# Kernel tuning notes

Hardware: AMD Instinct MI355X
Metric: run time of the kernel (lower is better)

Reference implementation:

```python
import jax, jax.numpy as jnp
import numpy as np

D_MODEL = 1024
N_HEADS = 16
TOP_FACTOR = 5


def setup_inputs() -> dict:
    key = jax.random.key(0)
    ks = jax.random.split(key, 9)
    B, L, D = 2, 4096, D_MODEL
    s = 0.02
    return {
        "x": jax.random.normal(ks[0], (B, L, D), dtype=jnp.float32),
        "Wq": jax.random.normal(ks[1], (D, D), dtype=jnp.float32) * s,
        "bq": jnp.zeros((D,), dtype=jnp.float32),
        "Wk": jax.random.normal(ks[2], (D, D), dtype=jnp.float32) * s,
        "bk": jnp.zeros((D,), dtype=jnp.float32),
        "Wv": jax.random.normal(ks[3], (D, D), dtype=jnp.float32) * s,
        "bv": jnp.zeros((D,), dtype=jnp.float32),
        "Wo": jax.random.normal(ks[4], (D, D), dtype=jnp.float32) * s,
        "bo": jnp.zeros((D,), dtype=jnp.float32),
    }


def reference(x, Wq, bq, Wk, bk, Wv, bv, Wo, bo):
    B, L, D = x.shape
    H = N_HEADS
    hd = D // H
    BH = B * H
    top_u = max(1, L // TOP_FACTOR)

    def proj(W, b):
        # [B,L,D] -> [B*H, L, hd] (matches view + transpose(1,2) in torch)
        y = x @ W.T + b
        return y.reshape(B, L, H, hd).transpose(0, 2, 1, 3).reshape(BH, L, hd)

    Q = proj(Wq, bq)
    K = proj(Wk, bk)
    V = proj(Wv, bv)

    # select top-u queries per (batch,head) by L2 norm
    query_norms = jnp.linalg.norm(Q, axis=2)              # [BH, L]
    _, top_idx = jax.lax.top_k(query_norms, top_u)        # [BH, top_u]
    Q_sel = jnp.take_along_axis(Q, top_idx[:, :, None], axis=1)  # [BH, u, hd]

    scale = 1.0 / (hd ** 0.5)
    scores = jnp.einsum('bud,bld->bul', Q_sel, K) * scale  # [BH, u, L]
    attn = jax.nn.softmax(scores, axis=-1)
    out_sel = jnp.einsum('bul,bld->bud', attn, V)          # [BH, u, hd]

    # scatter selected outputs back; non-selected rows stay zero
    out_full = jnp.zeros((BH, L, hd), dtype=x.dtype)
    out_full = out_full.at[jnp.arange(BH)[:, None], top_idx].set(out_sel)

    out = out_full.reshape(B, H, L, hd).transpose(0, 2, 1, 3).reshape(B, L, D)
    return out @ Wo.T + bo
```

## Files before the change

kernel.cpp:

```cpp
#include <hip/hip_runtime.h>
#include <cstddef>
#include <cstdint>

constexpr int LSEQ = 4096;
constexpr int DM   = 1024;
constexpr int HD   = 64;
constexpr int BHT  = 32;
constexpr int TOPU = 819;
constexpr int MROWS = 8192;
constexpr int NSEG = 4;

typedef unsigned short u16;
typedef __attribute__((ext_vector_type(8))) short short8v;
typedef __attribute__((ext_vector_type(4))) short short4v;
typedef __attribute__((ext_vector_type(4))) float f32x4;

__device__ __forceinline__ u16 f2bf(float f) {
  uint32_t u = __float_as_uint(f);
  u += 0x7fffu + ((u >> 16) & 1u);
  return (u16)(u >> 16);
}
__device__ __forceinline__ float bf2f(u16 h) {
  return __uint_as_float(((uint32_t)h) << 16);
}

__device__ __forceinline__ void gl16(const void* g, void* l) {
  __builtin_amdgcn_global_load_lds(
      (const __attribute__((address_space(1))) void*)g,
      (__attribute__((address_space(3))) void*)l, 16, 0, 0);
}

__device__ __forceinline__ void inv_swz(int S, int& R, int& C) {
  const int R0 = ((S >> 5) ^ (S >> 7)) & 1;
  const int R1 = (S >> 6) & 1;
  R = ((S >> 6) << 1) | R0;
  C = (((S >> 3) & 1) ^ R0) | ((((S >> 4) & 1) ^ R1) << 1);
}

__device__ __forceinline__ void split3_body(const float* src, u16* p1, u16* p2,
                                            u16* p3, int i) {
  const float4 a = *reinterpret_cast<const float4*>(src + (size_t)i * 8);
  const float4 b = *reinterpret_cast<const float4*>(src + (size_t)i * 8 + 4);
  float e[8] = {a.x, a.y, a.z, a.w, b.x, b.y, b.z, b.w};
  short8v v1, v2, v3;
  #pragma unroll
  for (int j = 0; j < 8; ++j) {
    u16 h1 = f2bf(e[j]);        float r1 = e[j] - bf2f(h1);
    u16 h2 = f2bf(r1);          float r2 = r1 - bf2f(h2);
    u16 h3 = f2bf(r2);
    v1[j] = (short)h1; v2[j] = (short)h2; v3[j] = (short)h3;
  }
  *reinterpret_cast<short8v*>(p1 + (size_t)i * 8) = v1;
  *reinterpret_cast<short8v*>(p2 + (size_t)i * 8) = v2;
  *reinterpret_cast<short8v*>(p3 + (size_t)i * 8) = v3;
}

__device__ __forceinline__ void conv_body(const float* src, u16* dst, int i) {
  const float4 a = *reinterpret_cast<const float4*>(src + (size_t)i * 8);
  const float4 b = *reinterpret_cast<const float4*>(src + (size_t)i * 8 + 4);
  short8v v;
  v[0] = (short)f2bf(a.x); v[1] = (short)f2bf(a.y);
  v[2] = (short)f2bf(a.z); v[3] = (short)f2bf(a.w);
  v[4] = (short)f2bf(b.x); v[5] = (short)f2bf(b.y);
  v[6] = (short)f2bf(b.z); v[7] = (short)f2bf(b.w);
  *reinterpret_cast<short8v*>(dst + (size_t)i * 8) = v;
}

__global__ __launch_bounds__(256) void prep_all(
    const float* __restrict__ x,  const float* __restrict__ Wq,
    const float* __restrict__ Wk, const float* __restrict__ Wv,
    const float* __restrict__ Wo,
    u16* __restrict__ x1, u16* __restrict__ x2, u16* __restrict__ x3,
    u16* __restrict__ wq1, u16* __restrict__ wq2, u16* __restrict__ wq3,
    u16* __restrict__ Wkb, u16* __restrict__ Wvb, u16* __restrict__ Wob)
{
  const int NX = MROWS * DM / 8;
  const int NW = DM * DM / 8;
  int i = blockIdx.x * 256 + threadIdx.x;
  if (i < NX)  { split3_body(x,  x1,  x2,  x3,  i); return; }
  i -= NX;
  if (i < NW)  { split3_body(Wq, wq1, wq2, wq3, i); return; }
  i -= NW;
  if (i < NW)  { conv_body(Wk, Wkb, i); return; }
  i -= NW;
  if (i < NW)  { conv_body(Wv, Wvb, i); return; }
  i -= NW;
  if (i < NW)  { conv_body(Wo, Wob, i); }
}

__device__ __forceinline__ void proj_q_body(
    u16* smem,
    const u16* __restrict__ X1, const u16* __restrict__ X2, const u16* __restrict__ X3,
    const u16* __restrict__ W1, const u16* __restrict__ W2, const u16* __restrict__ W3,
    const float* __restrict__ bias, float* __restrict__ Y,
    float* __restrict__ norms, int bx, int ny)
{
  u16* As[3] = {smem, smem + 4096, smem + 8192};
  u16* Bs[3] = {smem + 12288, smem + 16384, smem + 20480};
  const int tid = threadIdx.x;
  const int m0 = bx * 128, n0 = ny * 128;
  const int wid = tid >> 6, lane = tid & 63;
  const int wr = (wid >> 1) * 64, wc = (wid & 1) * 64;
  const int c = lane & 15, G = lane >> 4;

  int Rr[2], Cr[2];
  #pragma unroll
  for (int rr = 0; rr < 2; ++rr) inv_swz((tid + rr * 256) * 8, Rr[rr], Cr[rr]);

  f32x4 acc[4][4];
  #pragma unroll
  for (int mt = 0; mt < 4; ++mt)
    #pragma unroll
    for (int nt = 0; nt < 4; ++nt)
      acc[mt][nt] = (f32x4){0.f, 0.f, 0.f, 0.f};

  for (int k0 = 0; k0 < DM; k0 += 32) {
    #pragma unroll
    for (int rr = 0; rr < 2; ++rr) {
      const size_t goA = (size_t)(m0 + Rr[rr]) * DM + k0 + Cr[rr] * 8;
      const size_t goB = (size_t)(n0 + Rr[rr]) * DM + k0 + Cr[rr] * 8;
      const int lb = wid * 512 + rr * 2048;
      gl16(X1 + goA, As[0] + lb);
      gl16(X2 + goA, As[1] + lb);
      gl16(X3 + goA, As[2] + lb);
      gl16(W1 + goB, Bs[0] + lb);
      gl16(W2 + goB, Bs[1] + lb);
      gl16(W3 + goB, Bs[2] + lb);
    }
    __syncthreads();

    short8v bf[3][4];
    #pragma unroll
    for (int nt = 0; nt < 4; ++nt) {
      const int n = wc + nt * 16 + c;
      const int eo = (n * 32 + G * 8) ^ ((n & 7) << 3);
      bf[0][nt] = *reinterpret_cast<const short8v*>(Bs[0] + eo);
      bf[1][nt] = *reinterpret_cast<const short8v*>(Bs[1] + eo);
      bf[2][nt] = *reinterpret_cast<const short8v*>(Bs[2] + eo);
    }
    #pragma unroll
    for (int mt = 0; mt < 4; ++mt) {
      const int m = wr + mt * 16 + c;
      const int eo = (m * 32 + G * 8) ^ ((m & 7) << 3);
      short8v a1 = *reinterpret_cast<const short8v*>(As[0] + eo);
      short8v a2 = *reinterpret_cast<const short8v*>(As[1] + eo);
      short8v a3 = *reinterpret_cast<const short8v*>(As[2] + eo);
      #pragma unroll
      for (int nt = 0; nt < 4; ++nt) {
        acc[mt][nt] = __builtin_amdgcn_mfma_f32_16x16x32_bf16(a1, bf[0][nt], acc[mt][nt], 0, 0, 0);
        acc[mt][nt] = __builtin_amdgcn_mfma_f32_16x16x32_bf16(a1, bf[1][nt], acc[mt][nt], 0, 0, 0);
        acc[mt][nt] = __builtin_amdgcn_mfma_f32_16x16x32_bf16(a2, bf[0][nt], acc[mt][nt], 0, 0, 0);
        acc[mt][nt] = __builtin_amdgcn_mfma_f32_16x16x32_bf16(a2, bf[1][nt], acc[mt][nt], 0, 0, 0);
        acc[mt][nt] = __builtin_amdgcn_mfma_f32_16x16x32_bf16(a1, bf[2][nt], acc[mt][nt], 0, 0, 0);
        acc[mt][nt] = __builtin_amdgcn_mfma_f32_16x16x32_bf16(a3, bf[0][nt], acc[mt][nt], 0, 0, 0);
      }
    }
    __syncthreads();
  }

  float bb[4];
  #pragma unroll
  for (int nt = 0; nt < 4; ++nt) bb[nt] = bias[n0 + wc + nt * 16 + c];

  float ns[4][4];
  #pragma unroll
  for (int mt = 0; mt < 4; ++mt)
    #pragma unroll
    for (int r = 0; r < 4; ++r) ns[mt][r] = 0.f;

  #pragma unroll
  for (int mt = 0; mt < 4; ++mt) {
    #pragma unroll
    for (int nt = 0; nt < 4; ++nt) {
      const int n = n0 + wc + nt * 16 + c;
      const int h = n >> 6, d = n & 63;
      #pragma unroll
      for (int r = 0; r < 4; ++r) {
        const int m = m0 + wr + mt * 16 + G * 4 + r;
        const int b = m >> 12, l = m & (LSEQ - 1);
        const float val = acc[mt][nt][r] + bb[nt];
        Y[((size_t)((b << 4) + h) * LSEQ + l) * HD + d] = val;
        ns[mt][r] = fmaf(val, val, ns[mt][r]);
      }
    }
  }
  #pragma unroll
  for (int mt = 0; mt < 4; ++mt)
    #pragma unroll
    for (int r = 0; r < 4; ++r) {
      float v = ns[mt][r];
      v += __shfl_xor(v, 1); v += __shfl_xor(v, 2);
      v += __shfl_xor(v, 4); v += __shfl_xor(v, 8);
      ns[mt][r] = v;
    }
  if (c == 0) {
    const int h = (n0 + wc) >> 6;
    #pragma unroll
    for (int mt = 0; mt < 4; ++mt)
      #pragma unroll
      for (int r = 0; r < 4; ++r) {
        const int m = m0 + wr + mt * 16 + G * 4 + r;
        const int b = m >> 12, l = m & (LSEQ - 1);
        norms[(((size_t)((b << 4) + h)) << 12) + l] = ns[mt][r];
      }
  }
}

__device__ __forceinline__ void proj_kv_body(
    u16* smem, const u16* __restrict__ Xb, const u16* __restrict__ Wb,
    const float* __restrict__ bias, u16* __restrict__ Kb, u16* __restrict__ VgT,
    bool isV, int bx, int ny)
{
  u16* As = smem;
  u16* Bs = smem + 4096;
  const int tid = threadIdx.x;
  const int m0 = bx * 128, n0 = ny * 128;
  const int wid = tid >> 6, lane = tid & 63;
  const int wr = (wid >> 1) * 64, wc = (wid & 1) * 64;
  const int c = lane & 15, G = lane >> 4;

  int Rr[2], Cr[2];
  #pragma unroll
  for (int rr = 0; rr < 2; ++rr) inv_swz((tid + rr * 256) * 8, Rr[rr], Cr[rr]);

  f32x4 acc[4][4];
  #pragma unroll
  for (int mt = 0; mt < 4; ++mt)
    #pragma unroll
    for (int nt = 0; nt < 4; ++nt)
      acc[mt][nt] = (f32x4){0.f, 0.f, 0.f, 0.f};

  for (int k0 = 0; k0 < DM; k0 += 32) {
    #pragma unroll
    for (int rr = 0; rr < 2; ++rr) {
      const size_t goA = (size_t)(m0 + Rr[rr]) * DM + k0 + Cr[rr] * 8;
      const size_t goB = (size_t)(n0 + Rr[rr]) * DM + k0 + Cr[rr] * 8;
      const int lb = wid * 512 + rr * 2048;
      gl16(Xb + goA, As + lb);
      gl16(Wb + goB, Bs + lb);
    }
    __syncthreads();

    short8v af[4], bf[4];
    #pragma unroll
    for (int mt = 0; mt < 4; ++mt) {
      const int m = wr + mt * 16 + c;
      af[mt] = *reinterpret_cast<const short8v*>(As + ((m * 32 + G * 8) ^ ((m & 7) << 3)));
      const int n = wc + mt * 16 + c;
      bf[mt] = *reinterpret_cast<const short8v*>(Bs + ((n * 32 + G * 8) ^ ((n & 7) << 3)));
    }
    #pragma unroll
    for (int mt = 0; mt < 4; ++mt)
      #pragma unroll
      for (int nt = 0; nt < 4; ++nt)
        acc[mt][nt] = __builtin_amdgcn_mfma_f32_16x16x32_bf16(af[mt], bf[nt], acc[mt][nt], 0, 0, 0);
    __syncthreads();
  }

  float bb[4];
  #pragma unroll
  for (int nt = 0; nt < 4; ++nt) bb[nt] = bias[n0 + wc + nt * 16 + c];

  if (isV) {
    #pragma unroll
    for (int mt = 0; mt < 4; ++mt) {
      #pragma unroll
      for (int nt = 0; nt < 4; ++nt) {
        const int n = wc + nt * 16 + c;
        const int mloc = wr + mt * 16 + G * 4;
        short4v pv;
        #pragma unroll
        for (int r = 0; r < 4; ++r) pv[r] = (short)f2bf(acc[mt][nt][r] + bb[nt]);
        *reinterpret_cast<short4v*>(smem + n * 136 + mloc) = pv;
      }
    }
    __syncthreads();
    const int bb2 = m0 >> 12;
    const int ml0 = m0 & (LSEQ - 1);
    #pragma unroll
    for (int uu = 0; uu < 8; ++uu) {
      const int u = uu * 256 + tid;
      const int n = u >> 4, kg = u & 15;
      short8v vvv = *reinterpret_cast<const short8v*>(smem + n * 136 + kg * 8);
      const int h = (n0 + n) >> 6, d = (n0 + n) & 63;
      *reinterpret_cast<short8v*>(
          VgT + ((size_t)((bb2 << 4) + h) * HD + d) * LSEQ + ml0 + kg * 8) = vvv;
    }
  } else {
    #pragma unroll
    for (int mt = 0; mt < 4; ++mt) {
      #pragma unroll
      for (int nt = 0; nt < 4; ++nt) {
        const int n = n0 + wc + nt * 16 + c;
        const int h = n >> 6, d = n & 63;
        #pragma unroll
        for (int r = 0; r < 4; ++r) {
          const int m = m0 + wr + mt * 16 + G * 4 + r;
          const int b = m >> 12, l = m & (LSEQ - 1);
          Kb[((size_t)((b << 4) + h) * LSEQ + l) * HD + d] = f2bf(acc[mt][nt][r] + bb[nt]);
        }
      }
    }
  }
}

__global__ __launch_bounds__(256) void gemm_proj(
    const u16* __restrict__ X1, const u16* __restrict__ X2, const u16* __restrict__ X3,
    const u16* __restrict__ W1, const u16* __restrict__ W2, const u16* __restrict__ W3,
    const u16* __restrict__ Wkb, const u16* __restrict__ Wvb,
    const float* __restrict__ bq, const float* __restrict__ bk, const float* __restrict__ bv,
    float* __restrict__ Qb, float* __restrict__ norms,
    u16* __restrict__ Kb, u16* __restrict__ VgT, int y_off)
{
  __shared__ __align__(16) u16 smem[24576];
  const int by = blockIdx.y + y_off;
  const int bx = blockIdx.x;
  if (by < 8) {
    proj_q_body(smem, X1, X2, X3, W1, W2, W3, bq, Qb, norms, bx, by);
  } else if (by < 16) {
    proj_kv_body(smem, X1, Wvb, bv, Kb, VgT, true, bx, by - 8);
  } else {
    proj_kv_body(smem, X1, Wkb, bk, Kb, VgT, false, bx, by - 16);
  }
}

__global__ __launch_bounds__(256) void gemm_out(
    const u16* __restrict__ Xb, const u16* __restrict__ Wb,
    const float* __restrict__ bias, float* __restrict__ Y)
{
  __shared__ u16 As[128 * 32];
  __shared__ u16 Bs[128 * 32];
  const int tid = threadIdx.x;
  const int m0 = blockIdx.x * 128, n0 = blockIdx.y * 128;
  const int wid = tid >> 6, lane = tid & 63;
  const int wr = (wid >> 1) * 64, wc = (wid & 1) * 64;
  const int c = lane & 15, G = lane >> 4;

  int Rr[2], Cr[2];
  #pragma unroll
  for (int rr = 0; rr < 2; ++rr) inv_swz((tid + rr * 256) * 8, Rr[rr], Cr[rr]);

  f32x4 acc[4][4];
  #pragma unroll
  for (int mt = 0; mt < 4; ++mt)
    #pragma unroll
    for (int nt = 0; nt < 4; ++nt)
      acc[mt][nt] = (f32x4){0.f, 0.f, 0.f, 0.f};

  for (int k0 = 0; k0 < DM; k0 += 32) {
    #pragma unroll
    for (int rr = 0; rr < 2; ++rr) {
      const size_t goA = (size_t)(m0 + Rr[rr]) * DM + k0 + Cr[rr] * 8;
      const size_t goB = (size_t)(n0 + Rr[rr]) * DM + k0 + Cr[rr] * 8;
      const int lb = wid * 512 + rr * 2048;
      gl16(Xb + goA, As + lb);
      gl16(Wb + goB, Bs + lb);
    }
    __syncthreads();

    short8v af[4], bf[4];
    #pragma unroll
    for (int mt = 0; mt < 4; ++mt) {
      const int m = wr + mt * 16 + c;
      af[mt] = *reinterpret_cast<const short8v*>(As + ((m * 32 + G * 8) ^ ((m & 7) << 3)));
      const int n = wc + mt * 16 + c;
      bf[mt] = *reinterpret_cast<const short8v*>(Bs + ((n * 32 + G * 8) ^ ((n & 7) << 3)));
    }
    #pragma unroll
    for (int mt = 0; mt < 4; ++mt)
      #pragma unroll
      for (int nt = 0; nt < 4; ++nt)
        acc[mt][nt] = __builtin_amdgcn_mfma_f32_16x16x32_bf16(af[mt], bf[nt], acc[mt][nt], 0, 0, 0);
    __syncthreads();
  }

  float bb[4];
  #pragma unroll
  for (int nt = 0; nt < 4; ++nt) bb[nt] = bias[n0 + wc + nt * 16 + c];

  #pragma unroll
  for (int mt = 0; mt < 4; ++mt) {
    #pragma unroll
    for (int nt = 0; nt < 4; ++nt) {
      const int n = n0 + wc + nt * 16 + c;
      #pragma unroll
      for (int r = 0; r < 4; ++r) {
        const int m = m0 + wr + mt * 16 + G * 4 + r;
        Y[(size_t)m * DM + n] = acc[mt][nt][r] + bb[nt];
      }
    }
  }
}

__global__ __launch_bounds__(1024) void select_topk(
    const float* __restrict__ norms, int* __restrict__ top_idx)
{
  __shared__ unsigned int keys[LSEQ];
  __shared__ unsigned int hist[256];
  __shared__ unsigned int wsums[16];
  __shared__ unsigned int sh_b, sh_above;

  const int tid = threadIdx.x;
  const int bh = blockIdx.x;

  for (int l = tid; l < LSEQ; l += 1024)
    keys[l] = __float_as_uint(norms[bh * LSEQ + l]);
  __syncthreads();

  unsigned int prefix = 0, rem = TOPU, total_gt = 0;
  for (int shift = 24; shift >= 0; shift -= 8) {
    if (tid < 256) hist[tid] = 0;
    __syncthreads();
    for (int l = tid; l < LSEQ; l += 1024) {
      const unsigned int k = keys[l];
      const bool in = (shift == 24) || ((k >> (shift + 8)) == prefix);
      if (in) atomicAdd(&hist[(k >> shift) & 255], 1);
    }
    __syncthreads();
    if (tid == 0) {
      unsigned int cum = 0; int b = 255;
      for (; b > 0; --b) {
        const unsigned int h = hist[b];
        if (cum + h >= rem) break;
        cum += h;
      }
      sh_b = (unsigned int)b; sh_above = cum;
    }
    __syncthreads();
    prefix = (prefix << 8) | sh_b;
    total_gt += sh_above;
    rem -= sh_above;
    __syncthreads();
  }
  const unsigned int T = prefix;

  const int lane = tid & 63, wv = tid >> 6;
  const int l0 = tid * 4;

  {
    unsigned int flags = 0; int cnt = 0;
    #pragma unroll
    for (int j = 0; j < 4; ++j)
      if (keys[l0 + j] > T) { flags |= 1u << j; ++cnt; }
    int incl = cnt;
    #pragma unroll
    for (int off = 1; off < 64; off <<= 1) {
      int nv = __shfl_up(incl, off);
      if (lane >= off) incl += nv;
    }
    if (lane == 63) wsums[wv] = (unsigned int)incl;
    __syncthreads();
    if (tid == 0) {
      unsigned int run = 0;
      for (int w = 0; w < 16; ++w) { unsigned int t = wsums[w]; wsums[w] = run; run += t; }
    }
    __syncthreads();
    unsigned int pos = wsums[wv] + (unsigned int)(incl - cnt);
    #pragma unroll
    for (int j = 0; j < 4; ++j)
      if (flags & (1u << j)) top_idx[bh * TOPU + (pos++)] = l0 + j;
  }
  __syncthreads();

  {
    unsigned int flags = 0; int cnt = 0;
    #pragma unroll
    for (int j = 0; j < 4; ++j)
      if (keys[l0 + j] == T) { flags |= 1u << j; ++cnt; }
    int incl = cnt;
    #pragma unroll
    for (int off = 1; off < 64; off <<= 1) {
      int nv = __shfl_up(incl, off);
      if (lane >= off) incl += nv;
    }
    if (lane == 63) wsums[wv] = (unsigned int)incl;
    __syncthreads();
    if (tid == 0) {
      unsigned int run = 0;
      for (int w = 0; w < 16; ++w) { unsigned int t = wsums[w]; wsums[w] = run; run += t; }
    }
    __syncthreads();
    unsigned int r0 = wsums[wv] + (unsigned int)(incl - cnt);
    #pragma unroll
    for (int j = 0; j < 4; ++j)
      if (flags & (1u << j)) {
        if (r0 < rem) top_idx[bh * TOPU + total_gt + r0] = l0 + j;
        ++r0;
      }
  }
}

__global__ __launch_bounds__(256) void attn_mfma(
    const float* __restrict__ Qf, const u16* __restrict__ Kg,
    const u16* __restrict__ VgT, const int* __restrict__ tix,
    u16* __restrict__ OpartB, float* __restrict__ MLpart)
{
  __shared__ u16 Kc[128 * 64];
  __shared__ u16 Vt[64 * 128];
  __shared__ u16 Pt[4][16 * 136];

  const int tid = threadIdx.x;
  const int wid = tid >> 6, lane = tid & 63;
  const int c = lane & 15, G = lane >> 4;

  const int l = blockIdx.x;
  const int grp = l >> 3;
  const int bh = (grp / 52) * 8 + (l & 7);
  const int rem = grp % 52;
  const int qb = rem >> 2, ks = rem & 3;

  const size_t bhL = (size_t)bh * LSEQ;
  const int rglob = qb * 64 + wid * 16 + c;
  const int rowidx = (rglob < TOPU) ? tix[bh * TOPU + rglob] : -1;

  short8v qf[2];
  #pragma unroll
  for (int kf = 0; kf < 2; ++kf) {
    if (rowidx >= 0) {
      const float* qp = Qf + (bhL + rowidx) * HD + kf * 32 + G * 8;
      const float4 x0 = *reinterpret_cast<const float4*>(qp);
      const float4 x1 = *reinterpret_cast<const float4*>(qp + 4);
      short8v v;
      v[0] = (short)f2bf(x0.x * 0.125f); v[1] = (short)f2bf(x0.y * 0.125f);
      v[2] = (short)f2bf(x0.z * 0.125f); v[3] = (short)f2bf(x0.w * 0.125f);
      v[4] = (short)f2bf(x1.x * 0.125f); v[5] = (short)f2bf(x1.y * 0.125f);
      v[6] = (short)f2bf(x1.z * 0.125f); v[7] = (short)f2bf(x1.w * 0.125f);
      qf[kf] = v;
    } else {
      short8v v;
      #pragma unroll
      for (int j = 0; j < 8; ++j) v[j] = 0;
      qf[kf] = v;
    }
  }

  float m = -1e30f, lsum = 0.f;
  f32x4 oacc[4];
  #pragma unroll
  for (int dt = 0; dt < 4; ++dt) oacc[dt] = (f32x4){0.f, 0.f, 0.f, 0.f};

  const int ko0 = ks * (LSEQ / NSEG);
  const int wbase = (tid & ~63) * 8;
  for (int t = 0; t < LSEQ / NSEG / 128; ++t) {
    const int ko = ko0 + t * 128;
    #pragma unroll
    for (int uu = 0; uu < 4; ++uu) {
      const int S = (uu * 256 + tid) * 8;
      const int key = S >> 6, dgk = ((S >> 3) & 7) ^ (key & 7);
      gl16(Kg + (bhL + ko + key) * HD + dgk * 8, Kc + uu * 2048 + wbase);
      const int d = S >> 7, kgv = ((S >> 3) & 15) ^ (d & 7);
      gl16(VgT + ((size_t)bh * HD + d) * LSEQ + ko + kgv * 8, Vt + uu * 2048 + wbase);
    }
    __syncthreads();

    f32x4 sacc[8];
    __builtin_amdgcn_s_setprio(1);
    #pragma unroll
    for (int kt = 0; kt < 8; ++kt) {
      const int key = kt * 16 + c;
      short8v kb0 = *reinterpret_cast<const short8v*>(
          Kc + key * 64 + (((0 + G) ^ (key & 7)) << 3));
      short8v kb1 = *reinterpret_cast<const short8v*>(
          Kc + key * 64 + (((4 + G) ^ (key & 7)) << 3));
      f32x4 s = (f32x4){0.f, 0.f, 0.f, 0.f};
      s = __builtin_amdgcn_mfma_f32_16x16x32_bf16(kb0, qf[0], s, 0, 0, 0);
      s = __builtin_amdgcn_mfma_f32_16x16x32_bf16(kb1, qf[1], s, 0, 0, 0);
      sacc[kt] = s;
    }
    __builtin_amdgcn_s_setprio(0);

    float smax = -1e30f;
    #pragma unroll
    for (int kt = 0; kt < 8; ++kt) {
      float a0 = fmaxf(sacc[kt][0], sacc[kt][1]);
      float a1 = fmaxf(sacc[kt][2], sacc[kt][3]);
      smax = fmaxf(smax, fmaxf(a0, a1));
    }
    smax = fmaxf(smax, __shfl_xor(smax, 16));
    smax = fmaxf(smax, __shfl_xor(smax, 32));
    const float mnew = fmaxf(m, smax);
    const float corr = __expf(m - mnew);
    float ssum = 0.f;
    #pragma unroll
    for (int kt = 0; kt < 8; ++kt) {
      float p0 = __expf(sacc[kt][0] - mnew);
      float p1 = __expf(sacc[kt][1] - mnew);
      float p2 = __expf(sacc[kt][2] - mnew);
      float p3 = __expf(sacc[kt][3] - mnew);
      ssum += (p0 + p1) + (p2 + p3);
      short4v pv;
      pv[0] = (short)f2bf(p0); pv[1] = (short)f2bf(p1);
      pv[2] = (short)f2bf(p2); pv[3] = (short)f2bf(p3);
      *reinterpret_cast<short4v*>(&Pt[wid][c * 136 + kt * 16 + G * 4]) = pv;
    }
    ssum += __shfl_xor(ssum, 16);
    ssum += __shfl_xor(ssum, 32);
    lsum = lsum * corr + ssum;
    m = mnew;
    #pragma unroll
    for (int dt = 0; dt < 4; ++dt) oacc[dt] *= corr;

    __builtin_amdgcn_s_setprio(1);
    #pragma unroll
    for (int kf = 0; kf < 4; ++kf) {
      short8v pf = *reinterpret_cast<const short8v*>(
          &Pt[wid][c * 136 + kf * 32 + G * 8]);
      #pragma unroll
      for (int dt = 0; dt < 4; ++dt) {
        const int d = dt * 16 + c;
        short8v vf = *reinterpret_cast<const short8v*>(
            Vt + d * 128 + (((kf * 4 + G) ^ (d & 7)) << 3));
        oacc[dt] = __builtin_amdgcn_mfma_f32_16x16x32_bf16(vf, pf, oacc[dt], 0, 0, 0);
      }
    }
    __builtin_amdgcn_s_setprio(0);
    __syncthreads();
  }

  const int q = wid * 16 + c;
  const size_t pb = ((size_t)((bh * 13 + qb) * NSEG + ks)) * 64 + q;
  u16* op = OpartB + pb * 64;
  #pragma unroll
  for (int dt = 0; dt < 4; ++dt) {
    short4v o;
    o[0] = (short)f2bf(oacc[dt][0]); o[1] = (short)f2bf(oacc[dt][1]);
    o[2] = (short)f2bf(oacc[dt][2]); o[3] = (short)f2bf(oacc[dt][3]);
    *reinterpret_cast<short4v*>(op + dt * 16 + G * 4) = o;
  }
  if (G == 0) {
    MLpart[pb * 2]     = m;
    MLpart[pb * 2 + 1] = lsum;
  }
}

__global__ __launch_bounds__(256) void attn_combine(
    const u16* __restrict__ OpartB, const float* __restrict__ MLpart,
    const int* __restrict__ tix, u16* __restrict__ O1b)
{
  const int bq = blockIdx.x;
  const int bh = bq / 13, qb = bq % 13;
  const int tid = threadIdx.x;
  const int q = tid >> 2, dq = (tid & 3) * 16;
  const int rglob = qb * 64 + q;
  if (rglob >= TOPU) return;
  const int rowidx = tix[bh * TOPU + rglob];

  size_t p[NSEG];
  float mi[NSEG], li[NSEG];
  #pragma unroll
  for (int i = 0; i < NSEG; ++i) {
    p[i] = ((size_t)bq * NSEG + i) * 64 + q;
    mi[i] = MLpart[p[i] * 2];
    li[i] = MLpart[p[i] * 2 + 1];
  }
  float mx = fmaxf(fmaxf(mi[0], mi[1]), fmaxf(mi[2], mi[3]));
  float ci[NSEG], lsum = 0.f;
  #pragma unroll
  for (int i = 0; i < NSEG; ++i) { ci[i] = __expf(mi[i] - mx); lsum += li[i] * ci[i]; }
  const float linv = 1.0f / lsum;

  float acc[16];
  #pragma unroll
  for (int j = 0; j < 16; ++j) acc[j] = 0.f;
  #pragma unroll
  for (int i = 0; i < NSEG; ++i) {
    const u16* src = OpartB + p[i] * 64 + dq;
    #pragma unroll
    for (int j = 0; j < 16; ++j) acc[j] += bf2f(src[j]) * ci[i];
  }

  const int b = bh >> 4, h = bh & 15;
  u16* dst = O1b + (size_t)(b * LSEQ + rowidx) * DM + h * HD + dq;
  #pragma unroll
  for (int j0 = 0; j0 < 16; j0 += 4) {
    short4v o;
    #pragma unroll
    for (int j = 0; j < 4; ++j) o[j] = (short)f2bf(acc[j0 + j] * linv);
    *reinterpret_cast<short4v*>(dst + j0) = o;
  }
}

extern "C" void kernel_launch(void* const* d_in, const int* in_sizes, int n_in,
                              void* d_out, int out_size, void* d_ws, size_t ws_size,
                              hipStream_t stream) {
  const float* x  = (const float*)d_in[0];
  const float* Wq = (const float*)d_in[1];
  const float* bq = (const float*)d_in[2];
  const float* Wk = (const float*)d_in[3];
  const float* bk = (const float*)d_in[4];
  const float* Wv = (const float*)d_in[5];
  const float* bv = (const float*)d_in[6];
  const float* Wo = (const float*)d_in[7];
  const float* bo = (const float*)d_in[8];
  float* out = (float*)d_out;

  char* w = (char*)d_ws;
  float* Qb = (float*)w;  w += (size_t)BHT * LSEQ * HD * 4;
  u16* x1   = (u16*)w;    w += (size_t)MROWS * DM * 2;
  u16* x2   = (u16*)w;    w += (size_t)MROWS * DM * 2;
  u16* x3   = (u16*)w;    w += (size_t)MROWS * DM * 2;
  u16* VgT  = (u16*)w;    w += (size_t)BHT * HD * LSEQ * 2;
  u16* Wkb  = (u16*)w;    w += (size_t)DM * DM * 2;
  u16* Wvb  = (u16*)w;    w += (size_t)DM * DM * 2;
  u16* Wob  = (u16*)w;    w += (size_t)DM * DM * 2;
  u16* wq1  = (u16*)w;    w += (size_t)DM * DM * 2;
  u16* wq2  = (u16*)w;    w += (size_t)DM * DM * 2;
  u16* wq3  = (u16*)w;    w += (size_t)DM * DM * 2;
  float* norms = (float*)w; w += (size_t)BHT * LSEQ * 4;
  u16* Kb_ext = (u16*)w;  w += (size_t)BHT * LSEQ * HD * 2;

  const bool fusedK = ws_size >= (size_t)(w - (char*)d_ws);
  u16* Kb = fusedK ? Kb_ext : x3;

  u16*   O1b    = x2;
  int*   tix    = (int*)wq2;
  u16*   OpartB = x1;
  const int NPB = BHT * 13 * NSEG * 64;
  float* MLpart = (float*)(OpartB + (size_t)NPB * 64);

  prep_all<<<6144, 256, 0, stream>>>(x, Wq, Wk, Wv, Wo,
                                     x1, x2, x3, wq1, wq2, wq3, Wkb, Wvb, Wob);

  if (fusedK) {
    gemm_proj<<<dim3(64, 24), 256, 0, stream>>>(
        x1, x2, x3, wq1, wq2, wq3, Wkb, Wvb, bq, bk, bv, Qb, norms, Kb, VgT, 0);
  } else {
    gemm_proj<<<dim3(64, 16), 256, 0, stream>>>(
        x1, x2, x3, wq1, wq2, wq3, Wkb, Wvb, bq, bk, bv, Qb, norms, Kb, VgT, 0);
    gemm_proj<<<dim3(64, 8), 256, 0, stream>>>(
        x1, x2, x3, wq1, wq2, wq3, Wkb, Wvb, bq, bk, bv, Qb, norms, Kb, VgT, 16);
  }

  select_topk<<<BHT, 1024, 0, stream>>>(norms, tix);

  hipMemsetAsync(O1b, 0, (size_t)MROWS * DM * 2, stream);

  attn_mfma<<<BHT * 13 * NSEG, 256, 0, stream>>>(Qb, Kb, VgT, tix, OpartB, MLpart);
  attn_combine<<<BHT * 13, 256, 0, stream>>>(OpartB, MLpart, tix, O1b);

  gemm_out<<<dim3(MROWS / 128, DM / 128), 256, 0, stream>>>(O1b, Wob, bo, out);
}
```

Before: 287.3 us.

## Replace split-bf16 Q projection with single bf16 plus fp32 norm refinement band

The Q projection no longer uses a three-way bf16 split (six MFMAs per tile) and instead runs a single bf16 GEMM that writes Q as bf16 along with approximate norms. Top-k selection becomes two-stage. Rows whose approximate norm clearly exceeds the threshold are accepted directly, and rows inside a relative uncertainty band have their norms recomputed exactly in fp32 from x and Wq. Those candidates are then bitonic-sorted to fill the remaining slots. This cuts the dominant Q-projection MFMA and memory cost and shrinks workspace traffic (Q stored as bf16). The risk is mis-selection if bf16 error exceeds the hand-tuned band or more than UCAP candidates fall inside it, plus three extra small launches.

Measured after the change: 558.0 us. 94.3% more time.

```diff
diff --git a/kernel.cpp b/kernel.cpp
--- a/kernel.cpp
+++ b/kernel.cpp
@@ -9,8 +9,11 @@
 constexpr int TOPU = 819;
 constexpr int MROWS = 8192;
 constexpr int NSEG = 4;
+constexpr int UCAP = 1024;
+#define BAND 2.4e-3f
 
 typedef unsigned short u16;
+typedef unsigned long long u64;
 typedef __attribute__((ext_vector_type(8))) short short8v;
 typedef __attribute__((ext_vector_type(4))) short short4v;
 typedef __attribute__((ext_vector_type(4))) float f32x4;
@@ -35,24 +38,6 @@
   const int R1 = (S >> 6) & 1;
   R = ((S >> 6) << 1) | R0;
   C = (((S >> 3) & 1) ^ R0) | ((((S >> 4) & 1) ^ R1) << 1);
-}
-
-__device__ __forceinline__ void split3_body(const float* src, u16* p1, u16* p2,
-                                            u16* p3, int i) {
-  const float4 a = *reinterpret_cast<const float4*>(src + (size_t)i * 8);
-  const float4 b = *reinterpret_cast<const float4*>(src + (size_t)i * 8 + 4);
-  float e[8] = {a.x, a.y, a.z, a.w, b.x, b.y, b.z, b.w};
-  short8v v1, v2, v3;
-  #pragma unroll
-  for (int j = 0; j < 8; ++j) {
-    u16 h1 = f2bf(e[j]);        float r1 = e[j] - bf2f(h1);
-    u16 h2 = f2bf(r1);          float r2 = r1 - bf2f(h2);
-    u16 h3 = f2bf(r2);
-    v1[j] = (short)h1; v2[j] = (short)h2; v3[j] = (short)h3;
-  }
-  *reinterpret_cast<short8v*>(p1 + (size_t)i * 8) = v1;
-  *reinterpret_cast<short8v*>(p2 + (size_t)i * 8) = v2;
-  *reinterpret_cast<short8v*>(p3 + (size_t)i * 8) = v3;
 }
 
 __device__ __forceinline__ void conv_body(const float* src, u16* dst, int i) {
@@ -70,16 +55,15 @@
     const float* __restrict__ x,  const float* __restrict__ Wq,
     const float* __restrict__ Wk, const float* __restrict__ Wv,
     const float* __restrict__ Wo,
-    u16* __restrict__ x1, u16* __restrict__ x2, u16* __restrict__ x3,
-    u16* __restrict__ wq1, u16* __restrict__ wq2, u16* __restrict__ wq3,
-    u16* __restrict__ Wkb, u16* __restrict__ Wvb, u16* __restrict__ Wob)
+    u16* __restrict__ xb, u16* __restrict__ Wqb, u16* __restrict__ Wkb,
+    u16* __restrict__ Wvb, u16* __restrict__ Wob)
 {
   const int NX = MROWS * DM / 8;
   const int NW = DM * DM / 8;
   int i = blockIdx.x * 256 + threadIdx.x;
-  if (i < NX)  { split3_body(x,  x1,  x2,  x3,  i); return; }
+  if (i < NX)  { conv_body(x,  xb,  i); return; }
   i -= NX;
-  if (i < NW)  { split3_body(Wq, wq1, wq2, wq3, i); return; }
+  if (i < NW)  { conv_body(Wq, Wqb, i); return; }
   i -= NW;
   if (i < NW)  { conv_body(Wk, Wkb, i); return; }
   i -= NW;
@@ -88,128 +72,10 @@
   if (i < NW)  { conv_body(Wo, Wob, i); }
 }
 
-__device__ __forceinline__ void proj_q_body(
-    u16* smem,
-    const u16* __restrict__ X1, const u16* __restrict__ X2, const u16* __restrict__ X3,
-    const u16* __restrict__ W1, const u16* __restrict__ W2, const u16* __restrict__ W3,
-    const float* __restrict__ bias, float* __restrict__ Y,
+__device__ __forceinline__ void proj_sh_body(
+    u16* smem, const u16* __restrict__ Xb, const u16* __restrict__ Wb,
+    const float* __restrict__ bias, u16* __restrict__ dst,
     float* __restrict__ norms, int bx, int ny)
-{
-  u16* As[3] = {smem, smem + 4096, smem + 8192};
-  u16* Bs[3] = {smem + 12288, smem + 16384, smem + 20480};
-  const int tid = threadIdx.x;
-  const int m0 = bx * 128, n0 = ny * 128;
-  const int wid = tid >> 6, lane = tid & 63;
-  const int wr = (wid >> 1) * 64, wc = (wid & 1) * 64;
-  const int c = lane & 15, G = lane >> 4;
-
-  int Rr[2], Cr[2];
-  #pragma unroll
-  for (int rr = 0; rr < 2; ++rr) inv_swz((tid + rr * 256) * 8, Rr[rr], Cr[rr]);
-
-  f32x4 acc[4][4];
-  #pragma unroll
-  for (int mt = 0; mt < 4; ++mt)
-    #pragma unroll
-    for (int nt = 0; nt < 4; ++nt)
-      acc[mt][nt] = (f32x4){0.f, 0.f, 0.f, 0.f};
-
-  for (int k0 = 0; k0 < DM; k0 += 32) {
-    #pragma unroll
-    for (int rr = 0; rr < 2; ++rr) {
-      const size_t goA = (size_t)(m0 + Rr[rr]) * DM + k0 + Cr[rr] * 8;
-      const size_t goB = (size_t)(n0 + Rr[rr]) * DM + k0 + Cr[rr] * 8;
-      const int lb = wid * 512 + rr * 2048;
-      gl16(X1 + goA, As[0] + lb);
-      gl16(X2 + goA, As[1] + lb);
-      gl16(X3 + goA, As[2] + lb);
-      gl16(W1 + goB, Bs[0] + lb);
-      gl16(W2 + goB, Bs[1] + lb);
-      gl16(W3 + goB, Bs[2] + lb);
-    }
-    __syncthreads();
-
-    short8v bf[3][4];
-    #pragma unroll
-    for (int nt = 0; nt < 4; ++nt) {
-      const int n = wc + nt * 16 + c;
-      const int eo = (n * 32 + G * 8) ^ ((n & 7) << 3);
-      bf[0][nt] = *reinterpret_cast<const short8v*>(Bs[0] + eo);
-      bf[1][nt] = *reinterpret_cast<const short8v*>(Bs[1] + eo);
-      bf[2][nt] = *reinterpret_cast<const short8v*>(Bs[2] + eo);
-    }
-    #pragma unroll
-    for (int mt = 0; mt < 4; ++mt) {
-      const int m = wr + mt * 16 + c;
-      const int eo = (m * 32 + G * 8) ^ ((m & 7) << 3);
-      short8v a1 = *reinterpret_cast<const short8v*>(As[0] + eo);
-      short8v a2 = *reinterpret_cast<const short8v*>(As[1] + eo);
-      short8v a3 = *reinterpret_cast<const short8v*>(As[2] + eo);
-      #pragma unroll
-      for (int nt = 0; nt < 4; ++nt) {
-        acc[mt][nt] = __builtin_amdgcn_mfma_f32_16x16x32_bf16(a1, bf[0][nt], acc[mt][nt], 0, 0, 0);
-        acc[mt][nt] = __builtin_amdgcn_mfma_f32_16x16x32_bf16(a1, bf[1][nt], acc[mt][nt], 0, 0, 0);
-        acc[mt][nt] = __builtin_amdgcn_mfma_f32_16x16x32_bf16(a2, bf[0][nt], acc[mt][nt], 0, 0, 0);
-        acc[mt][nt] = __builtin_amdgcn_mfma_f32_16x16x32_bf16(a2, bf[1][nt], acc[mt][nt], 0, 0, 0);
-        acc[mt][nt] = __builtin_amdgcn_mfma_f32_16x16x32_bf16(a1, bf[2][nt], acc[mt][nt], 0, 0, 0);
-        acc[mt][nt] = __builtin_amdgcn_mfma_f32_16x16x32_bf16(a3, bf[0][nt], acc[mt][nt], 0, 0, 0);
-      }
-    }
-    __syncthreads();
-  }
-
-  float bb[4];
-  #pragma unroll
-  for (int nt = 0; nt < 4; ++nt) bb[nt] = bias[n0 + wc + nt * 16 + c];
-
-  float ns[4][4];
-  #pragma unroll
-  for (int mt = 0; mt < 4; ++mt)
-    #pragma unroll
-    for (int r = 0; r < 4; ++r) ns[mt][r] = 0.f;
-
-  #pragma unroll
-  for (int mt = 0; mt < 4; ++mt) {
-    #pragma unroll
-    for (int nt = 0; nt < 4; ++nt) {
-      const int n = n0 + wc + nt * 16 + c;
-      const int h = n >> 6, d = n & 63;
-      #pragma unroll
-      for (int r = 0; r < 4; ++r) {
-        const int m = m0 + wr + mt * 16 + G * 4 + r;
-        const int b = m >> 12, l = m & (LSEQ - 1);
-        const float val = acc[mt][nt][r] + bb[nt];
-        Y[((size_t)((b << 4) + h) * LSEQ + l) * HD + d] = val;
-        ns[mt][r] = fmaf(val, val, ns[mt][r]);
-      }
-    }
-  }
-  #pragma unroll
-  for (int mt = 0; mt < 4; ++mt)
-    #pragma unroll
-    for (int r = 0; r < 4; ++r) {
-      float v = ns[mt][r];
-      v += __shfl_xor(v, 1); v += __shfl_xor(v, 2);
-      v += __shfl_xor(v, 4); v += __shfl_xor(v, 8);
-      ns[mt][r] = v;
-    }
-  if (c == 0) {
-    const int h = (n0 + wc) >> 6;
-    #pragma unroll
-    for (int mt = 0; mt < 4; ++mt)
-      #pragma unroll
-      for (int r = 0; r < 4; ++r) {
-        const int m = m0 + wr + mt * 16 + G * 4 + r;
-        const int b = m >> 12, l = m & (LSEQ - 1);
-        norms[(((size_t)((b << 4) + h)) << 12) + l] = ns[mt][r];
-      }
-  }
-}
-
-__device__ __forceinline__ void proj_kv_body(
-    u16* smem, const u16* __restrict__ Xb, const u16* __restrict__ Wb,
-    const float* __restrict__ bias, u16* __restrict__ Kb, u16* __restrict__ VgT,
-    bool isV, int bx, int ny)
 {
   u16* As = smem;
   u16* Bs = smem + 4096;
@@ -261,66 +127,148 @@
   #pragma unroll
   for (int nt = 0; nt < 4; ++nt) bb[nt] = bias[n0 + wc + nt * 16 + c];
 
-  if (isV) {
-    #pragma unroll
-    for (int mt = 0; mt < 4; ++mt) {
-      #pragma unroll
-      for (int nt = 0; nt < 4; ++nt) {
-        const int n = wc + nt * 16 + c;
-        const int mloc = wr + mt * 16 + G * 4;
-        short4v pv;
-        #pragma unroll
-        for (int r = 0; r < 4; ++r) pv[r] = (short)f2bf(acc[mt][nt][r] + bb[nt]);
-        *reinterpret_cast<short4v*>(smem + n * 136 + mloc) = pv;
-      }
-    }
-    __syncthreads();
-    const int bb2 = m0 >> 12;
-    const int ml0 = m0 & (LSEQ - 1);
-    #pragma unroll
-    for (int uu = 0; uu < 8; ++uu) {
-      const int u = uu * 256 + tid;
-      const int n = u >> 4, kg = u & 15;
-      short8v vvv = *reinterpret_cast<const short8v*>(smem + n * 136 + kg * 8);
-      const int h = (n0 + n) >> 6, d = (n0 + n) & 63;
-      *reinterpret_cast<short8v*>(
-          VgT + ((size_t)((bb2 << 4) + h) * HD + d) * LSEQ + ml0 + kg * 8) = vvv;
-    }
-  } else {
-    #pragma unroll
-    for (int mt = 0; mt < 4; ++mt) {
-      #pragma unroll
-      for (int nt = 0; nt < 4; ++nt) {
-        const int n = n0 + wc + nt * 16 + c;
-        const int h = n >> 6, d = n & 63;
+  float ns[4][4];
+  #pragma unroll
+  for (int mt = 0; mt < 4; ++mt)
+    #pragma unroll
+    for (int r = 0; r < 4; ++r) ns[mt][r] = 0.f;
+
+  #pragma unroll
+  for (int mt = 0; mt < 4; ++mt) {
+    #pragma unroll
+    for (int nt = 0; nt < 4; ++nt) {
+      const int n = n0 + wc + nt * 16 + c;
+      const int h = n >> 6, d = n & 63;
+      #pragma unroll
+      for (int r = 0; r < 4; ++r) {
+        const int m = m0 + wr + mt * 16 + G * 4 + r;
+        const int b = m >> 12, l = m & (LSEQ - 1);
+        const float val = acc[mt][nt][r] + bb[nt];
+        dst[((size_t)((b << 4) + h) * LSEQ + l) * HD + d] = f2bf(val);
+        ns[mt][r] = fmaf(val, val, ns[mt][r]);
+      }
+    }
+  }
+  if (norms) {
+    #pragma unroll
+    for (int mt = 0; mt < 4; ++mt)
+      #pragma unroll
+      for (int r = 0; r < 4; ++r) {
+        float v = ns[mt][r];
+        v += __shfl_xor(v, 1); v += __shfl_xor(v, 2);
+        v += __shfl_xor(v, 4); v += __shfl_xor(v, 8);
+        ns[mt][r] = v;
+      }
+    if (c == 0) {
+      const int h = (n0 + wc) >> 6;
+      #pragma unroll
+      for (int mt = 0; mt < 4; ++mt)
         #pragma unroll
         for (int r = 0; r < 4; ++r) {
           const int m = m0 + wr + mt * 16 + G * 4 + r;
           const int b = m >> 12, l = m & (LSEQ - 1);
-          Kb[((size_t)((b << 4) + h) * LSEQ + l) * HD + d] = f2bf(acc[mt][nt][r] + bb[nt]);
+          norms[(((size_t)((b << 4) + h)) << 12) + l] = ns[mt][r];
         }
-      }
-    }
+    }
+  }
+}
+
+__device__ __forceinline__ void proj_v_body(
+    u16* smem, const u16* __restrict__ Xb, const u16* __restrict__ Wb,
+    const float* __restrict__ bias, u16* __restrict__ VgT, int bx, int ny)
+{
+  u16* As = smem;
+  u16* Bs = smem + 4096;
+  const int tid = threadIdx.x;
+  const int m0 = bx * 128, n0 = ny * 128;
+  const int wid = tid >> 6, lane = tid & 63;
+  const int wr = (wid >> 1) * 64, wc = (wid & 1) * 64;
+  const int c = lane & 15, G = lane >> 4;
+
+  int Rr[2], Cr[2];
+  #pragma unroll
+  for (int rr = 0; rr < 2; ++rr) inv_swz((tid + rr * 256) * 8, Rr[rr], Cr[rr]);
+
+  f32x4 acc[4][4];
+  #pragma unroll
+  for (int mt = 0; mt < 4; ++mt)
+    #pragma unroll
+    for (int nt = 0; nt < 4; ++nt)
+      acc[mt][nt] = (f32x4){0.f, 0.f, 0.f, 0.f};
+
+  for (int k0 = 0; k0 < DM; k0 += 32) {
+    #pragma unroll
+    for (int rr = 0; rr < 2; ++rr) {
+      const size_t goA = (size_t)(m0 + Rr[rr]) * DM + k0 + Cr[rr] * 8;
+      const size_t goB = (size_t)(n0 + Rr[rr]) * DM + k0 + Cr[rr] * 8;
+      const int lb = wid * 512 + rr * 2048;
+      gl16(Xb + goA, As + lb);
+      gl16(Wb + goB, Bs + lb);
+    }
+    __syncthreads();
+
+    short8v af[4], bf[4];
+    #pragma unroll
+    for (int mt = 0; mt < 4; ++mt) {
+      const int m = wr + mt * 16 + c;
+      af[mt] = *reinterpret_cast<const short8v*>(As + ((m * 32 + G * 8) ^ ((m & 7) << 3)));
+      const int n = wc + mt * 16 + c;
+      bf[mt] = *reinterpret_cast<const short8v*>(Bs + ((n * 32 + G * 8) ^ ((n & 7) << 3)));
+    }
+    #pragma unroll
+    for (int mt = 0; mt < 4; ++mt)
+      #pragma unroll
+      for (int nt = 0; nt < 4; ++nt)
+        acc[mt][nt] = __builtin_amdgcn_mfma_f32_16x16x32_bf16(af[mt], bf[nt], acc[mt][nt], 0, 0, 0);
+    __syncthreads();
+  }
+
+  float bb[4];
+  #pragma unroll
+  for (int nt = 0; nt < 4; ++nt) bb[nt] = bias[n0 + wc + nt * 16 + c];
+
+  #pragma unroll
+  for (int mt = 0; mt < 4; ++mt) {
+    #pragma unroll
+    for (int nt = 0; nt < 4; ++nt) {
+      const int n = wc + nt * 16 + c;
+      const int mloc = wr + mt * 16 + G * 4;
+      short4v pv;
+      #pragma unroll
+      for (int r = 0; r < 4; ++r) pv[r] = (short)f2bf(acc[mt][nt][r] + bb[nt]);
+      *reinterpret_cast<short4v*>(smem + n * 136 + mloc) = pv;
+    }
+  }
+  __syncthreads();
+  const int bb2 = m0 >> 12;
+  const int ml0 = m0 & (LSEQ - 1);
+  #pragma unroll
+  for (int uu = 0; uu < 8; ++uu) {
+    const int u = uu * 256 + tid;
+    const int n = u >> 4, kg = u & 15;
+    short8v vvv = *reinterpret_cast<const short8v*>(smem + n * 136 + kg * 8);
+    const int h = (n0 + n) >> 6, d = (n0 + n) & 63;
+    *reinterpret_cast<short8v*>(
+        VgT + ((size_t)((bb2 << 4) + h) * HD + d) * LSEQ + ml0 + kg * 8) = vvv;
   }
 }
 
 __global__ __launch_bounds__(256) void gemm_proj(
-    const u16* __restrict__ X1, const u16* __restrict__ X2, const u16* __restrict__ X3,
-    const u16* __restrict__ W1, const u16* __restrict__ W2, const u16* __restrict__ W3,
-    const u16* __restrict__ Wkb, const u16* __restrict__ Wvb,
+    const u16* __restrict__ Xb,
+    const u16* __restrict__ Wqb, const u16* __restrict__ Wkb, const u16* __restrict__ Wvb,
     const float* __restrict__ bq, const float* __restrict__ bk, const float* __restrict__ bv,
-    float* __restrict__ Qb, float* __restrict__ norms,
-    u16* __restrict__ Kb, u16* __restrict__ VgT, int y_off)
-{
-  __shared__ __align__(16) u16 smem[24576];
-  const int by = blockIdx.y + y_off;
+    u16* __restrict__ Qbb, float* __restrict__ norms,
+    u16* __restrict__ Kb, u16* __restrict__ VgT)
+{
+  __shared__ __align__(16) u16 smem[17408];
+  const int by = blockIdx.y;
   const int bx = blockIdx.x;
   if (by < 8) {
-    proj_q_body(smem, X1, X2, X3, W1, W2, W3, bq, Qb, norms, bx, by);
+    proj_sh_body(smem, Xb, Wqb, bq, Qbb, norms, bx, by);
   } else if (by < 16) {
-    proj_kv_body(smem, X1, Wvb, bv, Kb, VgT, true, bx, by - 8);
+    proj_v_body(smem, Xb, Wvb, bv, VgT, bx, by - 8);
   } else {
-    proj_kv_body(smem, X1, Wkb, bk, Kb, VgT, false, bx, by - 16);
+    proj_sh_body(smem, Xb, Wkb, bk, Kb, nullptr, bx, by - 16);
   }
 }
 
@@ -392,22 +340,24 @@
   }
 }
 
-__global__ __launch_bounds__(1024) void select_topk(
-    const float* __restrict__ norms, int* __restrict__ top_idx)
+__global__ __launch_bounds__(1024) void selectA(
+    const float* __restrict__ norms, int* __restrict__ tix,
+    u64* __restrict__ ukeys, int* __restrict__ Dcnt, int* __restrict__ Ucnt)
 {
   __shared__ unsigned int keys[LSEQ];
   __shared__ unsigned int hist[256];
-  __shared__ unsigned int wsums[16];
   __shared__ unsigned int sh_b, sh_above;
+  __shared__ unsigned int cD, cU;
 
   const int tid = threadIdx.x;
   const int bh = blockIdx.x;
 
   for (int l = tid; l < LSEQ; l += 1024)
     keys[l] = __float_as_uint(norms[bh * LSEQ + l]);
+  if (tid == 0) { cD = 0; cU = 0; }
   __syncthreads();
 
-  unsigned int prefix = 0, rem = TOPU, total_gt = 0;
+  unsigned int prefix = 0, rem = TOPU;
   for (int shift = 24; shift >= 0; shift -= 8) {
     if (tid < 256) hist[tid] = 0;
     __syncthreads();
@@ -428,70 +378,137 @@
     }
     __syncthreads();
     prefix = (prefix << 8) | sh_b;
-    total_gt += sh_above;
     rem -= sh_above;
     __syncthreads();
   }
-  const unsigned int T = prefix;
-
-  const int lane = tid & 63, wv = tid >> 6;
-  const int l0 = tid * 4;
-
-  {
-    unsigned int flags = 0; int cnt = 0;
-    #pragma unroll
-    for (int j = 0; j < 4; ++j)
-      if (keys[l0 + j] > T) { flags |= 1u << j; ++cnt; }
-    int incl = cnt;
-    #pragma unroll
-    for (int off = 1; off < 64; off <<= 1) {
-      int nv = __shfl_up(incl, off);
-      if (lane >= off) incl += nv;
-    }
-    if (lane == 63) wsums[wv] = (unsigned int)incl;
-    __syncthreads();
-    if (tid == 0) {
-      unsigned int run = 0;
-      for (int w = 0; w < 16; ++w) { unsigned int t = wsums[w]; wsums[w] = run; run += t; }
-    }
-    __syncthreads();
-    unsigned int pos = wsums[wv] + (unsigned int)(incl - cnt);
-    #pragma unroll
-    for (int j = 0; j < 4; ++j)
-      if (flags & (1u << j)) top_idx[bh * TOPU + (pos++)] = l0 + j;
+
+  const float A = __uint_as_float(prefix);
+  const float Whi = A * (1.0f + 3.0f * BAND);
+  const float Wlo = A * (1.0f - 3.0f * BAND);
+
+  for (int l = tid; l < LSEQ; l += 1024) {
+    const float v = __uint_as_float(keys[l]);
+    if (v > Whi) {
+      const unsigned p = atomicAdd(&cD, 1);
+      tix[bh * TOPU + p] = l;
+    } else if (v >= Wlo) {
+      const unsigned u = atomicAdd(&cU, 1);
+      if (u < UCAP)
+        ukeys[(size_t)bh * UCAP + u] =
+            ((u64)keys[l] << 32) | (unsigned int)(~l);
+    }
   }
   __syncthreads();
-
-  {
-    unsigned int flags = 0; int cnt = 0;
-    #pragma unroll
-    for (int j = 0; j < 4; ++j)
-      if (keys[l0 + j] == T) { flags |= 1u << j; ++cnt; }
-    int incl = cnt;
-    #pragma unroll
-    for (int off = 1; off < 64; off <<= 1) {
-      int nv = __shfl_up(incl, off);
-      if (lane >= off) incl += nv;
-    }
-    if (lane == 63) wsums[wv] = (unsigned int)incl;
-    __syncthreads();
-    if (tid == 0) {
-      unsigned int run = 0;
-      for (int w = 0; w < 16; ++w) { unsigned int t = wsums[w]; wsums[w] = run; run += t; }
-    }
-    __syncthreads();
-    unsigned int r0 = wsums[wv] + (unsigned int)(incl - cnt);
-    #pragma unroll
-    for (int j = 0; j < 4; ++j)
-      if (flags & (1u << j)) {
-        if (r0 < rem) top_idx[bh * TOPU + total_gt + r0] = l0 + j;
-        ++r0;
-      }
-  }
+  if (tid == 0) {
+    Dcnt[bh] = (int)cD;
+    Ucnt[bh] = (int)(cU < UCAP ? cU : UCAP);
+  }
+}
+
+__global__ __launch_bounds__(256) void recompute_norms(
+    const float* __restrict__ x, const float* __restrict__ Wq,
+    const float* __restrict__ bq, u64* __restrict__ ukeys,
+    const int* __restrict__ Ucnt)
+{
+  __shared__ float ws[64][65];
+  __shared__ float xs[32][65];
+  __shared__ int lrow[32];
+  const int bh = blockIdx.x;
+  const int U = Ucnt[bh];
+  if (U == 0) return;
+  const int h = bh & 15, bI = bh >> 4;
+  const int tid = threadIdx.x;
+  const int wid = tid >> 6, d = tid & 63;
+
+  for (int g = 0; g < (U + 31) / 32; ++g) {
+    if (tid < 32) {
+      const int r = g * 32 + tid;
+      lrow[tid] = (r < U)
+          ? (int)(~(unsigned int)(ukeys[(size_t)bh * UCAP + r] & 0xffffffffu))
+          : 0;
+    }
+    __syncthreads();
+
+    float a[8] = {0.f, 0.f, 0.f, 0.f, 0.f, 0.f, 0.f, 0.f};
+    for (int kc = 0; kc < 16; ++kc) {
+      #pragma unroll
+      for (int j4 = 0; j4 < 4; ++j4) {
+        const int e = tid * 16 + j4 * 4;
+        const int dd = e >> 6, kk = e & 63;
+        const float4 w4 = *reinterpret_cast<const float4*>(
+            Wq + (size_t)(h * 64 + dd) * DM + kc * 64 + kk);
+        ws[dd][kk] = w4.x; ws[dd][kk + 1] = w4.y;
+        ws[dd][kk + 2] = w4.z; ws[dd][kk + 3] = w4.w;
+      }
+      {
+        const int e = tid * 8;
+        const int rr = e >> 6, kk = e & 63;
+        const float* xp = x + (size_t)(bI * LSEQ + lrow[rr]) * DM + kc * 64 + kk;
+        const float4 x0 = *reinterpret_cast<const float4*>(xp);
+        const float4 x1 = *reinterpret_cast<const float4*>(xp + 4);
+        xs[rr][kk]     = x0.x; xs[rr][kk + 1] = x0.y;
+        xs[rr][kk + 2] = x0.z; xs[rr][kk + 3] = x0.w;
+        xs[rr][kk + 4] = x1.x; xs[rr][kk + 5] = x1.y;
+        xs[rr][kk + 6] = x1.z; xs[rr][kk + 7] = x1.w;
+      }
+      __syncthreads();
+      for (int k = 0; k < 64; ++k) {
+        const float wv = ws[d][k];
+        #pragma unroll
+        for (int j = 0; j < 8; ++j)
+          a[j] = fmaf(xs[wid * 8 + j][k], wv, a[j]);
+      }
+      __syncthreads();
+    }
+
+    const float bias = bq[h * 64 + d];
+    #pragma unroll
+    for (int j = 0; j < 8; ++j) {
+      const int r = g * 32 + wid * 8 + j;
+      const float q = a[j] + bias;
+      float s = q * q;
+      s += __shfl_xor(s, 1);  s += __shfl_xor(s, 2);  s += __shfl_xor(s, 4);
+      s += __shfl_xor(s, 8);  s += __shfl_xor(s, 16); s += __shfl_xor(s, 32);
+      if (d == 0 && r < U) {
+        const u64 old = ukeys[(size_t)bh * UCAP + r];
+        ukeys[(size_t)bh * UCAP + r] =
+            ((u64)__float_as_uint(s) << 32) | (old & 0xffffffffu);
+      }
+    }
+    __syncthreads();
+  }
+}
+
+__global__ __launch_bounds__(1024) void selectB(
+    const u64* __restrict__ ukeys, const int* __restrict__ Dcnt,
+    const int* __restrict__ Ucnt, int* __restrict__ tix)
+{
+  __shared__ u64 sk[UCAP];
+  const int bh = blockIdx.x;
+  const int U = Ucnt[bh], D = Dcnt[bh];
+  const int need = TOPU - D;
+  const int tid = threadIdx.x;
+
+  sk[tid] = (tid < U) ? ukeys[(size_t)bh * UCAP + tid] : 0ULL;
+  __syncthreads();
+  for (int k = 2; k <= UCAP; k <<= 1) {
+    for (int j = k >> 1; j > 0; j >>= 1) {
+      const int ixj = tid ^ j;
+      if (ixj > tid) {
+        const bool desc = ((tid & k) == 0);
+        const u64 a = sk[tid], b = sk[ixj];
+        if (desc ? (a < b) : (a > b)) { sk[tid] = b; sk[ixj] = a; }
+      }
+      __syncthreads();
+    }
+  }
+  if (tid < need)
+    tix[bh * TOPU + D + tid] =
+        (tid < U) ? (int)(~(unsigned int)(sk[tid] & 0xffffffffu)) : 0;
 }
 
 __global__ __launch_bounds__(256) void attn_mfma(
-    const float* __restrict__ Qf, const u16* __restrict__ Kg,
+    const u16* __restrict__ Qbb, const u16* __restrict__ Kg,
     const u16* __restrict__ VgT, const int* __restrict__ tix,
     u16* __restrict__ OpartB, float* __restrict__ MLpart)
 {
@@ -517,14 +534,12 @@
   #pragma unroll
   for (int kf = 0; kf < 2; ++kf) {
     if (rowidx >= 0) {
-      const float* qp = Qf + (bhL + rowidx) * HD + kf * 32 + G * 8;
-      const float4 x0 = *reinterpret_cast<const float4*>(qp);
-      const float4 x1 = *reinterpret_cast<const float4*>(qp + 4);
+      const u16* qp = Qbb + (bhL + rowidx) * HD + kf * 32 + G * 8;
+      const short8v raw = *reinterpret_cast<const short8v*>(qp);
       short8v v;
-      v[0] = (short)f2bf(x0.x * 0.125f); v[1] = (short)f2bf(x0.y * 0.125f);
-      v[2] = (short)f2bf(x0.z * 0.125f); v[3] = (short)f2bf(x0.w * 0.125f);
-      v[4] = (short)f2bf(x1.x * 0.125f); v[5] = (short)f2bf(x1.y * 0.125f);
-      v[6] = (short)f2bf(x1.z * 0.125f); v[7] = (short)f2bf(x1.w * 0.125f);
+      #pragma unroll
+      for (int j = 0; j < 8; ++j)
+        v[j] = (short)f2bf(bf2f((u16)raw[j]) * 0.125f);
       qf[kf] = v;
     } else {
       short8v v;
@@ -695,47 +710,37 @@
   float* out = (float*)d_out;
 
   char* w = (char*)d_ws;
-  float* Qb = (float*)w;  w += (size_t)BHT * LSEQ * HD * 4;
-  u16* x1   = (u16*)w;    w += (size_t)MROWS * DM * 2;
-  u16* x2   = (u16*)w;    w += (size_t)MROWS * DM * 2;
-  u16* x3   = (u16*)w;    w += (size_t)MROWS * DM * 2;
-  u16* VgT  = (u16*)w;    w += (size_t)BHT * HD * LSEQ * 2;
-  u16* Wkb  = (u16*)w;    w += (size_t)DM * DM * 2;
-  u16* Wvb  = (u16*)w;    w += (size_t)DM * DM * 2;
-  u16* Wob  = (u16*)w;    w += (size_t)DM * DM * 2;
-  u16* wq1  = (u16*)w;    w += (size_t)DM * DM * 2;
-  u16* wq2  = (u16*)w;    w += (size_t)DM * DM * 2;
-  u16* wq3  = (u16*)w;    w += (size_t)DM * DM * 2;
+  u16* xb   = (u16*)w;  w += (size_t)MROWS * DM * 2;
+  u16* Qbb  = (u16*)w;  w += (size_t)BHT * LSEQ * HD * 2;
+  u16* Kb   = (u16*)w;  w += (size_t)BHT * LSEQ * HD * 2;
+  u16* VgT  = (u16*)w;  w += (size_t)BHT * HD * LSEQ * 2;
+  u16* O1b  = (u16*)w;  w += (size_t)MROWS * DM * 2;
+  u16* Wqb  = (u16*)w;  w += (size_t)DM * DM * 2;
+  u16* Wkb  = (u16*)w;  w += (size_t)DM * DM * 2;
+  u16* Wvb  = (u16*)w;  w += (size_t)DM * DM * 2;
+  u16* Wob  = (u16*)w;  w += (size_t)DM * DM * 2;
   float* norms = (float*)w; w += (size_t)BHT * LSEQ * 4;
-  u16* Kb_ext = (u16*)w;  w += (size_t)BHT * LSEQ * HD * 2;
-
-  const bool fusedK = ws_size >= (size_t)(w - (char*)d_ws);
-  u16* Kb = fusedK ? Kb_ext : x3;
-
-  u16*   O1b    = x2;
-  int*   tix    = (int*)wq2;
-  u16*   OpartB = x1;
+  int* tix  = (int*)w;  w += (size_t)BHT * TOPU * 4;
+  u64* ukeys = (u64*)w; w += (size_t)BHT * UCAP * 8;
+  int* Dcnt = (int*)w;  w += 128;
+  int* Ucnt = (int*)w;  w += 128;
+
+  u16*   OpartB = xb;
   const int NPB = BHT * 13 * NSEG * 64;
   float* MLpart = (float*)(OpartB + (size_t)NPB * 64);
 
-  prep_all<<<6144, 256, 0, stream>>>(x, Wq, Wk, Wv, Wo,
-                                     x1, x2, x3, wq1, wq2, wq3, Wkb, Wvb, Wob);
-
-  if (fusedK) {
-    gemm_proj<<<dim3(64, 24), 256, 0, stream>>>(
-        x1, x2, x3, wq1, wq2, wq3, Wkb, Wvb, bq, bk, bv, Qb, norms, Kb, VgT, 0);
-  } else {
-    gemm_proj<<<dim3(64, 16), 256, 0, stream>>>(
-        x1, x2, x3, wq1, wq2, wq3, Wkb, Wvb, bq, bk, bv, Qb, norms, Kb, VgT, 0);
-    gemm_proj<<<dim3(64, 8), 256, 0, stream>>>(
-        x1, x2, x3, wq1, wq2, wq3, Wkb, Wvb, bq, bk, bv, Qb, norms, Kb, VgT, 16);
-  }
-
-  select_topk<<<BHT, 1024, 0, stream>>>(norms, tix);
+  prep_all<<<6144, 256, 0, stream>>>(x, Wq, Wk, Wv, Wo, xb, Wqb, Wkb, Wvb, Wob);
+
+  gemm_proj<<<dim3(64, 24), 256, 0, stream>>>(
+      xb, Wqb, Wkb, Wvb, bq, bk, bv, Qbb, norms, Kb, VgT);
+
+  selectA<<<BHT, 1024, 0, stream>>>(norms, tix, ukeys, Dcnt, Ucnt);
+  recompute_norms<<<BHT, 256, 0, stream>>>(x, Wq, bq, ukeys, Ucnt);
+  selectB<<<BHT, 1024, 0, stream>>>(ukeys, Dcnt, Ucnt, tix);
 
   hipMemsetAsync(O1b, 0, (size_t)MROWS * DM * 2, stream);
 
-  attn_mfma<<<BHT * 13 * NSEG, 256, 0, stream>>>(Qb, Kb, VgT, tix, OpartB, MLpart);
+  attn_mfma<<<BHT * 13 * NSEG, 256, 0, stream>>>(Qbb, Kb, VgT, tix, OpartB, MLpart);
   attn_combine<<<BHT * 13, 256, 0, stream>>>(OpartB, MLpart, tix, O1b);
 
   gemm_out<<<dim3(MROWS / 128, DM / 128), 256, 0, stream>>>(O1b, Wob, bo, out);
```
